# Kernel tuning notes

Hardware: AMD Instinct MI355X
Metric: run time of the kernel (lower is better)

## Reference

```python
import jax, jax.numpy as jnp
import numpy as np
from jax import lax

B_, L_, D_ = 4, 512, 512          # batch, seq_len, in_dim (d_model)
HID, H2 = 512, 256                # hidden_dim, per-direction LSTM width
NL, DST, DCV, DIN, DTR = 3, 16, 4, 1024, 32  # layers, d_state, d_conv, d_inner, dt_rank


def _silu(x):
    return x * jax.nn.sigmoid(x)


def _layernorm(x, g, b):
    m = x.mean(-1, keepdims=True)
    v = x.var(-1, keepdims=True)
    return (x - m) / jnp.sqrt(v + 1e-5) * g + b


def _mamba(x, wi, cw, cb, xpw, dw, db, Alog, Dp, wo):
    # x: (B,L,D)
    Bsz, Ls, _ = x.shape
    xz = jnp.einsum('bld,ed->ble', x, wi)          # (B,L,2*DIN)
    xin, z = jnp.split(xz, 2, axis=-1)
    # causal depthwise conv1d (kernel DCV, left-padded)
    xpad = jnp.pad(xin, ((0, 0), (DCV - 1, 0), (0, 0)))
    u = cb + sum(xpad[:, k:k + Ls, :] * cw[:, k] for k in range(DCV))
    u = _silu(u)                                   # (B,L,DIN)
    xdbl = jnp.einsum('blc,ec->ble', u, xpw)       # (B,L,DTR+2*DST)
    dt_in = xdbl[..., :DTR]
    Bc = xdbl[..., DTR:DTR + DST]
    Cc = xdbl[..., DTR + DST:]
    dt = jax.nn.softplus(jnp.einsum('blr,cr->blc', dt_in, dw) + db)  # (B,L,DIN)
    A = -jnp.exp(Alog)                             # (DIN,DST), negative

    def step(h, inp):
        dt_t, B_t, C_t, u_t = inp                  # (B,DIN),(B,DST),(B,DST),(B,DIN)
        dA = jnp.exp(dt_t[..., None] * A)          # (B,DIN,DST)
        h = dA * h + (dt_t * u_t)[..., None] * B_t[:, None, :]
        y = jnp.einsum('bcn,bn->bc', h, C_t)
        return h, y

    h0 = jnp.zeros((Bsz, DIN, DST), x.dtype)
    _, ys = lax.scan(step, h0, (dt.transpose(1, 0, 2), Bc.transpose(1, 0, 2),
                                Cc.transpose(1, 0, 2), u.transpose(1, 0, 2)))
    y = ys.transpose(1, 0, 2) + u * Dp
    y = y * _silu(z)
    return jnp.einsum('blc,dc->bld', y, wo)


def _lstm_dir(x, wih, whh, bih, bhh, reverse):
    Bsz = x.shape[0]

    def step(carry, xt):
        h, c = carry
        g = xt @ wih.T + h @ whh.T + bih + bhh     # (B,4*H2), PyTorch gate order i,f,g,o
        i, f, gg, o = jnp.split(g, 4, axis=-1)
        c = jax.nn.sigmoid(f) * c + jax.nn.sigmoid(i) * jnp.tanh(gg)
        h = jax.nn.sigmoid(o) * jnp.tanh(c)
        return (h, c), h

    init = (jnp.zeros((Bsz, H2), x.dtype), jnp.zeros((Bsz, H2), x.dtype))
    _, hs = lax.scan(step, init, x.transpose(1, 0, 2), reverse=reverse)
    return hs.transpose(1, 0, 2)


def setup_inputs():
    key = jax.random.key(0)
    ks = jax.random.split(key, 16)
    rn = lambda k, s, sc=0.02: jax.random.normal(k, s, jnp.float32) * sc
    inp = {}
    inp['x'] = jax.random.normal(ks[0], (B_, L_, D_), jnp.float32)
    inp['in_proj_w'] = rn(ks[1], (NL, 2 * DIN, D_))
    inp['conv_w'] = rn(ks[2], (NL, DIN, DCV), 0.2)
    inp['conv_b'] = jnp.zeros((NL, DIN), jnp.float32)
    inp['x_proj_w'] = rn(ks[3], (NL, DTR + 2 * DST, DIN))
    inp['dt_proj_w'] = rn(ks[4], (NL, DIN, DTR), 0.1)
    inp['dt_proj_b'] = jnp.full((NL, DIN), -4.0, jnp.float32)
    inp['A_log'] = jnp.log(jnp.broadcast_to(jnp.arange(1, DST + 1, dtype=jnp.float32), (NL, DIN, DST)))
    inp['D_param'] = jnp.ones((NL, DIN), jnp.float32)
    inp['out_proj_w'] = rn(ks[5], (NL, D_, DIN))
    inp['ln_g'] = jnp.ones((NL, D_), jnp.float32)
    inp['ln_b'] = jnp.zeros((NL, D_), jnp.float32)
    inp['lstm_w_ih'] = rn(ks[6], (2, 4 * H2, D_), 0.05)
    inp['lstm_w_hh'] = rn(ks[7], (2, 4 * H2, H2), 0.05)
    inp['lstm_b_ih'] = jnp.zeros((2, 4 * H2), jnp.float32)
    inp['lstm_b_hh'] = jnp.zeros((2, 4 * H2), jnp.float32)
    inp['fusion_w'] = rn(ks[8], (HID, D_ + HID), 0.02)
    inp['fusion_b'] = jnp.zeros((HID,), jnp.float32)
    return inp


def reference(x, in_proj_w, conv_w, conv_b, x_proj_w, dt_proj_w, dt_proj_b, A_log,
              D_param, out_proj_w, ln_g, ln_b, lstm_w_ih, lstm_w_hh, lstm_b_ih,
              lstm_b_hh, fusion_w, fusion_b):
    m = x
    for i in range(NL):
        mo = _mamba(m, in_proj_w[i], conv_w[i], conv_b[i], x_proj_w[i],
                    dt_proj_w[i], dt_proj_b[i], A_log[i], D_param[i], out_proj_w[i])
        m = _layernorm(m + mo, ln_g[i], ln_b[i])
    lf = _lstm_dir(x, lstm_w_ih[0], lstm_w_hh[0], lstm_b_ih[0], lstm_b_hh[0], False)
    lb = _lstm_dir(x, lstm_w_ih[1], lstm_w_hh[1], lstm_b_ih[1], lstm_b_hh[1], True)
    comb = jnp.concatenate([m, lf, lb], axis=-1)   # (B,L,D_+HID)
    return comb @ fusion_w.T + fusion_b
```

## Files before the change

### kernel.cpp

```cpp
#include <hip/hip_runtime.h>
#include <math.h>

#define B_  4
#define L_  512
#define D_  512
#define DIN 1024
#define DST 16
#define DCV 4
#define DTR 32
#define NL  3
#define H2  256
#define LCH 128
#define WSC 0.28f

typedef _Float16 __f16;
typedef __f16 f16x2 __attribute__((ext_vector_type(2)));
typedef __f16 half8 __attribute__((ext_vector_type(8)));
typedef float f32x4v __attribute__((ext_vector_type(4)));
typedef unsigned uint4v __attribute__((ext_vector_type(4)));

__device__ __forceinline__ float fast_sigmoid(float x) { return 1.f / (1.f + __expf(-x)); }
__device__ __forceinline__ float fast_tanh(float x) { return 2.f / (1.f + __expf(-2.f * x)) - 1.f; }

__device__ __forceinline__ float dot2f(unsigned a, unsigned b, float c) {
  return __builtin_amdgcn_fdot2(__builtin_bit_cast(f16x2, a),
                                __builtin_bit_cast(f16x2, b), c, false);
}
__device__ __forceinline__ unsigned packf16(float a, float b) {
  f16x2 p; p.x = (__f16)a; p.y = (__f16)b;
  return __builtin_bit_cast(unsigned, p);
}
__device__ __forceinline__ int sdot4(unsigned a, unsigned b, int c) {
  return __builtin_amdgcn_sdot4((int)a, (int)b, c, false);
}
__device__ __forceinline__ int q8(float v) {
  float c = fmaxf(fminf(v, 127.f), -127.f);
  return (int)rintf(c);
}

template<int ACT, bool ACC, bool HOUT>
__global__ __launch_bounds__(256) void gemm_mfma_h(
    const __f16* __restrict__ A, const __f16* __restrict__ W, void* __restrict__ Cv,
    int M, int N, int K, int lda, int ldb, int ldc,
    const float* __restrict__ bias, const float* __restrict__ bias2)
{
  __shared__ uint4v As[1024];
  __shared__ uint4v Bs[1024];
  const int tid  = threadIdx.x;
  const int lane = tid & 63, wid = tid >> 6;
  const int wr = wid >> 1, wc = wid & 1;
  const int fr = lane & 15, fq = lane >> 4;
  const int m0 = blockIdx.y * 128, n0 = blockIdx.x * 128;
  const int srow = tid >> 3, skb = tid & 7;

  f32x4v acc[4][4] = {};
  for (int k0 = 0; k0 < K; k0 += 64) {
    const __f16* Ab = A + (size_t)m0 * lda + k0;
    const __f16* Bb = W + (size_t)n0 * ldb + k0;
    #pragma unroll
    for (int i = 0; i < 4; ++i) {
      int row = srow + i * 32;
      uint4v ap = *(const uint4v*)(Ab + (size_t)row * lda + skb * 8);
      uint4v bp = *(const uint4v*)(Bb + (size_t)row * ldb + skb * 8);
      As[row * 8 + (skb ^ (row & 7))] = ap;
      Bs[row * 8 + (skb ^ (row & 7))] = bp;
    }
    __syncthreads();
    #pragma unroll
    for (int ks = 0; ks < 2; ++ks) {
      half8 af[4], bf[4];
      #pragma unroll
      for (int mt = 0; mt < 4; ++mt) {
        int row = wr * 64 + mt * 16 + fr;
        int kb = ks * 4 + fq;
        af[mt] = __builtin_bit_cast(half8, As[row * 8 + (kb ^ (row & 7))]);
      }
      #pragma unroll
      for (int nt = 0; nt < 4; ++nt) {
        int row = wc * 64 + nt * 16 + fr;
        int kb = ks * 4 + fq;
        bf[nt] = __builtin_bit_cast(half8, Bs[row * 8 + (kb ^ (row & 7))]);
      }
      #pragma unroll
      for (int mt = 0; mt < 4; ++mt)
        #pragma unroll
        for (int nt = 0; nt < 4; ++nt)
          acc[mt][nt] = __builtin_amdgcn_mfma_f32_16x16x32_f16(af[mt], bf[nt], acc[mt][nt], 0, 0, 0);
    }
    __syncthreads();
  }
  float* C = (float*)Cv;
  __f16* Ch = (__f16*)Cv;
  #pragma unroll
  for (int nt = 0; nt < 4; ++nt) {
    int n = n0 + wc * 64 + nt * 16 + fr;
    float bv = (bias ? bias[n] : 0.f) + (bias2 ? bias2[n] : 0.f);
    #pragma unroll
    for (int mt = 0; mt < 4; ++mt) {
      #pragma unroll
      for (int r = 0; r < 4; ++r) {
        int m = m0 + wr * 64 + mt * 16 + fq * 4 + r;
        float v = acc[mt][nt][r] + bv;
        if (ACT == 1) v = (v > 20.f) ? v : log1pf(__expf(v));
        if (HOUT) Ch[(size_t)m * ldc + n] = (__f16)v;
        else if (ACC) C[(size_t)m * ldc + n] += v;
        else C[(size_t)m * ldc + n] = v;
      }
    }
  }
}

__global__ __launch_bounds__(256) void packh(
    const float* __restrict__ src, __f16* __restrict__ dst, int n)
{
  int t = blockIdx.x * 256 + threadIdx.x;
  if (t < n) dst[t] = (__f16)src[t];
}

__global__ __launch_bounds__(256) void pack_xpw_h(
    const float* __restrict__ xpw, __f16* __restrict__ dst)
{
  int t = blockIdx.x * 256 + threadIdx.x;
  int layer = t >> 17;
  int r = (t >> 10) & 127;
  int k = t & 1023;
  dst[t] = (r < 64) ? (__f16)xpw[layer * 65536 + r * 1024 + k] : (__f16)0.f;
}

__global__ __launch_bounds__(256) void pack_dwh(
    const float* __restrict__ dw, __f16* __restrict__ dst)
{
  int t = blockIdx.x * 256 + threadIdx.x;
  int layer = t >> 16;
  int r = (t >> 6) & 1023;
  int k = t & 63;
  dst[t] = (k < 32) ? (__f16)dw[layer * 32768 + r * 32 + k] : (__f16)0.f;
}

__global__ __launch_bounds__(256) void pack_whh_i8(
    const float* __restrict__ whh, uint4* __restrict__ dst)
{
  int idx = blockIdx.x * 256 + threadIdx.x;
  int t = idx & 511;
  int q = (idx >> 9) & 7;
  int r = idx >> 12;
  int G = r % 3, dir = r / 3;
  int j = t >> 1, ks = t & 1;
  const float* src = whh + (size_t)dir * 262144 + (size_t)(G * 256 + j) * 256 + ks * 128 + q * 16;
  const float inv = 127.f / WSC;
  unsigned d[4];
  #pragma unroll
  for (int w = 0; w < 4; ++w) {
    float4 f = ((const float4*)src)[w];
    int q0 = q8(f.x * inv), q1 = q8(f.y * inv), q2 = q8(f.z * inv), q3 = q8(f.w * inv);
    d[w] = (unsigned)(q0 & 255) | ((unsigned)(q1 & 255) << 8) |
           ((unsigned)(q2 & 255) << 16) | ((unsigned)(q3 & 255) << 24);
  }
  uint4 pk; pk.x = d[0]; pk.y = d[1]; pk.z = d[2]; pk.w = d[3];
  dst[idx] = pk;
}

__global__ __launch_bounds__(256) void pack_whh_o(
    const float* __restrict__ whh, uint4* __restrict__ dst)
{
  int idx = blockIdx.x * 256 + threadIdx.x;
  int t = idx & 511;
  int q = (idx >> 9) & 15;
  int dir = idx >> 13;
  int j = t >> 1, ks = t & 1;
  const float* src = whh + (size_t)dir * 262144 + (size_t)(768 + j) * 256 + ks * 128 + q * 8;
  float4 fa = ((const float4*)src)[0];
  float4 fb = ((const float4*)src)[1];
  uint4 pk;
  pk.x = packf16(fa.x, fa.y); pk.y = packf16(fa.z, fa.w);
  pk.z = packf16(fb.x, fb.y); pk.w = packf16(fb.z, fb.w);
  dst[idx] = pk;
}

__global__ __launch_bounds__(256) void conv_silu(
    const float* __restrict__ xz, const float* __restrict__ cw, const float* __restrict__ cb,
    float* __restrict__ u, __f16* __restrict__ uh)
{
  int t = blockIdx.x * 256 + threadIdx.x;
  int c  = t & (DIN - 1);
  int bl = t >> 10;
  int l  = bl & (L_ - 1);
  float acc = cb[c];
  #pragma unroll
  for (int k = 0; k < DCV; ++k) {
    int ls = l + k - (DCV - 1);
    if (ls >= 0)
      acc = fmaf(xz[(size_t)(bl + k - (DCV - 1)) * 2048 + c], cw[c * DCV + k], acc);
  }
  float v = acc * fast_sigmoid(acc);
  u[t] = v;
  uh[t] = (__f16)v;
}

__global__ __launch_bounds__(256) void scan_part(
    const float* __restrict__ dt, const float* __restrict__ u,
    const __f16* __restrict__ xdh, const float* __restrict__ A_log,
    float* __restrict__ hend, float* __restrict__ Pp)
{
  int t = blockIdx.x * 256 + threadIdx.x;
  int n  = t & 15;
  int ch = (t >> 4) & 3;
  int bc = t >> 6;
  int c  = bc & (DIN - 1);
  int b  = bc >> 10;
  float Ac = -__expf(A_log[c * DST + n]);
  float h = 0.f, P = 1.f;
  const size_t row = (size_t)b * L_ + ch * LCH;

#define DECLP(i) float dtv##i, uv##i, Bn##i;
  DECLP(0) DECLP(1) DECLP(2) DECLP(3)
#define LOADP(i, l) { \
    const size_t nb_ = row + (l); \
    dtv##i = dt[nb_ * DIN + c]; \
    uv##i  = u [nb_ * DIN + c]; \
    Bn##i  = (float)xdh[nb_ * 128 + 32 + n]; }
#define STEPP(i) { \
    float dA_ = __expf(dtv##i * Ac); \
    h = fmaf(dA_, h, (dtv##i * uv##i) * Bn##i); \
    P *= dA_; }

  LOADP(0, 0) LOADP(1, 1) LOADP(2, 2) LOADP(3, 3)
  for (int l = 0; l < LCH - 4; l += 4) {
    STEPP(0) LOADP(0, l + 4)
    STEPP(1) LOADP(1, l + 5)
    STEPP(2) LOADP(2, l + 6)
    STEPP(3) LOADP(3, l + 7)
  }
  STEPP(0) STEPP(1) STEPP(2) STEPP(3)
#undef DECLP
#undef LOADP
#undef STEPP
  int flat = bc * 16 + n;
  hend[ch * 65536 + flat] = h;
  Pp[ch * 65536 + flat]   = P;
}

__global__ __launch_bounds__(256) void scan_fix(
    const float* __restrict__ dt, const float* __restrict__ u,
    const __f16* __restrict__ xdh, const float* __restrict__ xz,
    const float* __restrict__ A_log, const float* __restrict__ Dp,
    const float* __restrict__ hend, const float* __restrict__ Pp,
    __f16* __restrict__ y)
{
  int t = blockIdx.x * 256 + threadIdx.x;
  int n  = t & 15;
  int ch = (t >> 4) & 3;
  int bc = t >> 6;
  int c  = bc & (DIN - 1);
  int b  = bc >> 10;
  float Ac = -__expf(A_log[c * DST + n]);
  float Dc = Dp[c];
  const int flat = bc * 16 + n;
  float h = 0.f;
  if (ch > 0) h = hend[flat];
  if (ch > 1) h = fmaf(Pp[1 * 65536 + flat], h, hend[1 * 65536 + flat]);
  if (ch > 2) h = fmaf(Pp[2 * 65536 + flat], h, hend[2 * 65536 + flat]);
  const size_t row = (size_t)b * L_ + ch * LCH;

#define DECLP(i) float dtv##i, uv##i, Bn##i, Cn##i, zv##i;
  DECLP(0) DECLP(1) DECLP(2) DECLP(3)
#define LOADP(i, l) { \
    const size_t nb_ = row + (l); \
    dtv##i = dt[nb_ * DIN + c]; \
    uv##i  = u [nb_ * DIN + c]; \
    Bn##i  = (float)xdh[nb_ * 128 + 32 + n]; \
    Cn##i  = (float)xdh[nb_ * 128 + 48 + n]; \
    zv##i  = xz[nb_ * 2048 + 1024 + c]; }
#define STEPP(i, l) { \
    float dA_ = __expf(dtv##i * Ac); \
    h = fmaf(dA_, h, (dtv##i * uv##i) * Bn##i); \
    float p_ = h * Cn##i; \
    p_ += __shfl_xor(p_, 1, 64); \
    p_ += __shfl_xor(p_, 2, 64); \
    p_ += __shfl_xor(p_, 4, 64); \
    p_ += __shfl_xor(p_, 8, 64); \
    if (n == 0) { \
      float yv_ = p_ + uv##i * Dc; \
      yv_ *= zv##i * fast_sigmoid(zv##i); \
      y[(row + (l)) * DIN + c] = (__f16)yv_; \
    } }

  LOADP(0, 0) LOADP(1, 1) LOADP(2, 2) LOADP(3, 3)
  for (int l = 0; l < LCH - 4; l += 4) {
    STEPP(0, l)     LOADP(0, l + 4)
    STEPP(1, l + 1) LOADP(1, l + 5)
    STEPP(2, l + 2) LOADP(2, l + 6)
    STEPP(3, l + 3) LOADP(3, l + 7)
  }
  STEPP(0, LCH - 4) STEPP(1, LCH - 3) STEPP(2, LCH - 2) STEPP(3, LCH - 1)
#undef DECLP
#undef LOADP
#undef STEPP
}

__global__ __launch_bounds__(64) void resid_ln(
    const float* __restrict__ a, const float* __restrict__ mo,
    const float* __restrict__ g, const float* __restrict__ bta,
    float* __restrict__ outm, int ldo, __f16* __restrict__ outh, int ldoh)
{
  int row = blockIdx.x;
  int lane = threadIdx.x;
  const float* pa = a  + (size_t)row * 512;
  const float* pb = mo + (size_t)row * 512;
  float v[8];
  float s = 0.f, s2 = 0.f;
  #pragma unroll
  for (int i = 0; i < 8; ++i) {
    float x = pa[lane + i * 64] + pb[lane + i * 64];
    v[i] = x; s += x; s2 += x * x;
  }
  #pragma unroll
  for (int off = 1; off < 64; off <<= 1) {
    s  += __shfl_xor(s,  off, 64);
    s2 += __shfl_xor(s2, off, 64);
  }
  float mean = s * (1.f / 512.f);
  float var  = s2 * (1.f / 512.f) - mean * mean;
  float rstd = rsqrtf(var + 1e-5f);
  #pragma unroll
  for (int i = 0; i < 8; ++i) {
    int cidx = lane + i * 64;
    float o = (v[i] - mean) * rstd * g[cidx] + bta[cidx];
    if (outm) outm[(size_t)row * ldo + cidx] = o;
    outh[(size_t)row * ldoh + cidx] = (__f16)o;
  }
}


#define W8DECL(q) uint4 WI8_##q, WF8_##q, WG8_##q;
#define W8LOAD(q) WI8_##q = wp8[(0*8+(q))*512 + t]; \
                  WF8_##q = wp8[(1*8+(q))*512 + t]; \
                  WG8_##q = wp8[(2*8+(q))*512 + t];
#define W8STEP(q) { \
    uint4 hq = h8s[buf][(q)*2 + ks]; \
    ii_ = sdot4(WI8_##q.x, hq.x, ii_); ii_ = sdot4(WI8_##q.y, hq.y, ii_); \
    ii_ = sdot4(WI8_##q.z, hq.z, ii_); ii_ = sdot4(WI8_##q.w, hq.w, ii_); \
    if_ = sdot4(WF8_##q.x, hq.x, if_); if_ = sdot4(WF8_##q.y, hq.y, if_); \
    if_ = sdot4(WF8_##q.z, hq.z, if_); if_ = sdot4(WF8_##q.w, hq.w, if_); \
    ig_ = sdot4(WG8_##q.x, hq.x, ig_); ig_ = sdot4(WG8_##q.y, hq.y, ig_); \
    ig_ = sdot4(WG8_##q.z, hq.z, ig_); ig_ = sdot4(WG8_##q.w, hq.w, ig_); }
#define OSTEP(q) { \
    uint4 hv = h4s[buf][(q)*2 + ks]; \
    uint4 wv = wo_lds[(q)*512 + t]; \
    a3 = dot2f(wv.x, hv.x, a3); a3 = dot2f(wv.y, hv.y, a3); \
    a3 = dot2f(wv.z, hv.z, a3); a3 = dot2f(wv.w, hv.w, a3); }
#define REP8(M) M(0) M(1) M(2) M(3) M(4) M(5) M(6) M(7)
#define REP16(M) M(0) M(1) M(2) M(3) M(4) M(5) M(6) M(7) \
                 M(8) M(9) M(10) M(11) M(12) M(13) M(14) M(15)

__global__ __launch_bounds__(512, 1) void lstm_rec(
    const float* __restrict__ gx, const uint4* __restrict__ wpk8,
    const uint4* __restrict__ wpko, __f16* __restrict__ comb)
{
  __shared__ uint4 wo_lds[16 * 512];
  __shared__ __align__(16) uint4 h4s[2][32];
  __shared__ __align__(16) uint4 h8s[2][16];
  const int dir = blockIdx.x >> 2, b = blockIdx.x & 3;
  const int t = threadIdx.x;
  const int j = t >> 1, ks = t & 1;
  const uint4* wp8 = wpk8 + (size_t)dir * 3 * 8 * 512;
  const uint4* wpo = wpko + (size_t)dir * 16 * 512;
  const float WS = WSC / (127.f * 127.f);

  REP8(W8DECL)
  REP8(W8LOAD)

  #pragma unroll
  for (int q = 0; q < 16; ++q)
    wo_lds[q * 512 + t] = wpo[q * 512 + t];

  if (t < 256) ((unsigned*)h4s)[t] = 0u;
  if (t < 128) ((unsigned*)h8s)[t] = 0u;
  float c_reg = 0.f;
  __f16* outp = comb + 512 + dir * 256;
  const float* gxb = gx + (size_t)(b * L_) * 2048 + dir * 1024;
  const int offA = (ks ? 1 : 0) * 256 + j;
  const int offB = (ks ? 3 : 2) * 256 + j;
  const int p_   = t >> 2;
  const int hidx = ((p_ >> 2) & 15) * 8 + (p_ >> 6) * 4 + (p_ & 3);
  const int d_   = j >> 2;
  const int ks8  = d_ >> 5;
  const int h8i  = (((d_ - ks8 * 32) >> 2) * 2 + ks8) * 4 + (d_ & 3);
  __syncthreads();

  int buf = 0;
  const int l0 = dir ? (L_ - 1) : 0;
  float pgA = gxb[(size_t)l0 * 2048 + offA];
  float pgB = gxb[(size_t)l0 * 2048 + offB];

  for (int s = 0; s < L_; ++s) {
    const int l = dir ? (L_ - 1 - s) : s;
    float pgA_n = 0.f, pgB_n = 0.f;
    if (s + 1 < L_) {
      const int ln = dir ? (L_ - 2 - s) : (s + 1);
      pgA_n = gxb[(size_t)ln * 2048 + offA];
      pgB_n = gxb[(size_t)ln * 2048 + offB];
    }
    int ii_ = 0, if_ = 0, ig_ = 0;
    float a3 = 0.f;
    REP8(W8STEP)
    REP16(OSTEP)
    float a0 = (float)ii_ * WS;
    float a1 = (float)if_ * WS;
    float a2 = (float)ig_ * WS;
    if (ks == 0) { a0 += pgA; a2 += pgB; } else { a1 += pgA; a3 += pgB; }
    a0 += __shfl_xor(a0, 1, 64);
    a1 += __shfl_xor(a1, 1, 64);
    a2 += __shfl_xor(a2, 1, 64);
    a3 += __shfl_xor(a3, 1, 64);
    const float si = fast_sigmoid(a0);
    const float sf = fast_sigmoid(a1);
    const float tg = fast_tanh(a2);
    const float so = fast_sigmoid(a3);
    c_reg = fmaf(sf, c_reg, si * tg);
    const float hv = so * fast_tanh(c_reg);
    if (ks == 0) outp[(size_t)(b * L_ + l) * 1024 + j] = (__f16)hv;
    const float hv1 = __shfl_xor(hv, 2, 64);
    const float hv2 = __shfl_xor(hv, 4, 64);
    const float hv3 = __shfl_xor(hv1, 4, 64);
    if ((t & 3) == 0)
      ((unsigned*)h4s[buf ^ 1])[hidx] = packf16(hv, hv1);
    if ((t & 7) == 0) {
      int q0 = (int)rintf(hv  * 127.f), q1 = (int)rintf(hv1 * 127.f);
      int q2 = (int)rintf(hv2 * 127.f), q3 = (int)rintf(hv3 * 127.f);
      ((unsigned*)h8s[buf ^ 1])[h8i] =
          (unsigned)(q0 & 255) | ((unsigned)(q1 & 255) << 8) |
          ((unsigned)(q2 & 255) << 16) | ((unsigned)(q3 & 255) << 24);
    }
    pgA = pgA_n; pgB = pgB_n;
    buf ^= 1;
    __syncthreads();
  }
}

extern "C" void kernel_launch(void* const* d_in, const int* in_sizes, int n_in,
                              void* d_out, int out_size, void* d_ws, size_t ws_size,
                              hipStream_t stream)
{
  const float* x    = (const float*)d_in[0];
  const float* wi   = (const float*)d_in[1];
  const float* cw   = (const float*)d_in[2];
  const float* cb   = (const float*)d_in[3];
  const float* xpw  = (const float*)d_in[4];
  const float* dw   = (const float*)d_in[5];
  const float* db   = (const float*)d_in[6];
  const float* Alog = (const float*)d_in[7];
  const float* Dp   = (const float*)d_in[8];
  const float* wo   = (const float*)d_in[9];
  const float* lng  = (const float*)d_in[10];
  const float* lnb  = (const float*)d_in[11];
  const float* wih  = (const float*)d_in[12];
  const float* whh  = (const float*)d_in[13];
  const float* bih  = (const float*)d_in[14];
  const float* bhh  = (const float*)d_in[15];
  const float* fw   = (const float*)d_in[16];
  const float* fb   = (const float*)d_in[17];
  float* out = (float*)d_out;

  float* F = (float*)d_ws;
  float* xz     = F;
  float* gx     = F;
  float* mo     = F + 3145728;
  float* u      = F + 4194304;
  __f16* xdh    = (__f16*)(F + 7340032);
  float* dt     = F + 7602176;
  float* mbuf   = F + 10747904;
  __f16* fw_h   = (__f16*)(F + 4194304);
  __f16* u_h    = (__f16*)(F + 6291456);
  __f16* wih_h  = (__f16*)(F + 7602176);
  uint4* wpk8   = (uint4*)(F + 8126464);
  uint4* wpko   = (uint4*)(F + 8224768);
  __f16* wi_hc  = (__f16*)(F + 8388608);
  __f16* ybuf_h = (__f16*)(F + 9699328);
  __f16* x_h    = (__f16*)(F + 9699328);
  __f16* mbuf_h = (__f16*)(F + 11796480);
  __f16* comb_h = (__f16*)(F + 12320768);
  __f16* wo_h   = (__f16*)(F + 13369344);
  __f16* xpw_h  = (__f16*)(F + 14155776);
  __f16* dwh    = (__f16*)(F + 14352384);
  float* hend   = F + 14450688;
  float* Pp     = F + 14712832;

  const int M = B_ * L_;
  dim3 blk(256);

  packh<<<dim3(4096), blk, 0, stream>>>(x,   x_h,   1048576);
  packh<<<dim3(4096), blk, 0, stream>>>(wih, wih_h, 1048576);
  packh<<<dim3(6144), blk, 0, stream>>>(wo,  wo_h,  1572864);
  pack_xpw_h<<<dim3(1536), blk, 0, stream>>>(xpw, xpw_h);
  pack_dwh<<<dim3(768), blk, 0, stream>>>(dw, dwh);

  gemm_mfma_h<0,false,false><<<dim3(16, 16), blk, 0, stream>>>(
      x_h, wih_h, gx, M, 2048, 512, 512, 512, 2048, bih, bhh);
  pack_whh_i8<<<dim3(96), blk, 0, stream>>>(whh, wpk8);
  pack_whh_o<<<dim3(64), blk, 0, stream>>>(whh, wpko);
  lstm_rec<<<dim3(8), dim3(512), 0, stream>>>(gx, wpk8, wpko, comb_h);

  for (int i = 0; i < NL; ++i) {
    const float* min = (i == 0) ? x : mbuf;
    const __f16* min_h = (i == 0) ? x_h : mbuf_h;
    packh<<<dim3(4096), blk, 0, stream>>>(wi + (size_t)i*1048576, wi_hc, 1048576);
    gemm_mfma_h<0,false,false><<<dim3(16, 16), blk, 0, stream>>>(
        min_h, wi_hc, xz, M, 2048, 512, 512, 512, 2048, nullptr, nullptr);
    conv_silu<<<dim3(8192), blk, 0, stream>>>(
        xz, cw + (size_t)i*DIN*DCV, cb + i*DIN, u, u_h);
    gemm_mfma_h<0,false,true><<<dim3(1, 16), blk, 0, stream>>>(
        u_h, xpw_h + (size_t)i*131072, xdh, M, 128, 1024, 1024, 1024, 128, nullptr, nullptr);
    gemm_mfma_h<1,false,false><<<dim3(8, 16), blk, 0, stream>>>(
        xdh, dwh + (size_t)i*65536, dt, M, 1024, 64, 128, 64, 1024, db + i*1024, nullptr);
    scan_part<<<dim3(1024), blk, 0, stream>>>(
        dt, u, xdh, Alog + (size_t)i*DIN*DST, hend, Pp);
    scan_fix<<<dim3(1024), blk, 0, stream>>>(
        dt, u, xdh, xz, Alog + (size_t)i*DIN*DST, Dp + i*DIN, hend, Pp, ybuf_h);
    gemm_mfma_h<0,false,false><<<dim3(4, 16), blk, 0, stream>>>(
        ybuf_h, wo_h + (size_t)i*524288, mo, M, 512, 1024, 1024, 1024, 512, nullptr, nullptr);
    if (i < NL - 1)
      resid_ln<<<dim3(M), dim3(64), 0, stream>>>(
          min, mo, lng + i*512, lnb + i*512, mbuf, 512, mbuf_h, 512);
    else
      resid_ln<<<dim3(M), dim3(64), 0, stream>>>(
          min, mo, lng + i*512, lnb + i*512, nullptr, 0, comb_h, 1024);
  }

  packh<<<dim3(2048), blk, 0, stream>>>(fw, fw_h, 524288);
  gemm_mfma_h<0,false,false><<<dim3(4, 16), blk, 0, stream>>>(
      comb_h, fw_h, out, M, 512, 1024, 1024, 1024, 512, fb, nullptr);
}
```

Before: 1.347 ms.

## Quantize LSTM output gate to int8 and split Mamba scan into eight chunks

The LSTM recurrence now uses int8 weights for the output gate too, so it goes through the same sdot4 path as the other gates. This drops the separate fp16 hidden-state buffer, its pack kernel and the 16 fp16 dot2 steps per timestep, and halves the LDS weight footprint. Separately, the selective scan is split into 8 chunks of 64 instead of 4 of 128, doubling the parallelism in scan_part and scan_fix, at the cost of a longer serial prefix combine and workspace relocation for hend and Pp. The added int8 quantization of the output-gate weights may reduce accuracy.

Result: faster. 1.292 ms (-4.1%).

```diff
diff --git a/kernel.cpp b/kernel.cpp
--- a/kernel.cpp
+++ b/kernel.cpp
@@ -10,7 +10,8 @@
 #define DTR 32
 #define NL  3
 #define H2  256
-#define LCH 128
+#define LCH 64
+#define NCH 8
 #define WSC 0.28f
 
 typedef _Float16 __f16;
@@ -144,7 +145,7 @@
   int t = idx & 511;
   int q = (idx >> 9) & 7;
   int r = idx >> 12;
-  int G = r % 3, dir = r / 3;
+  int G = r & 3, dir = r >> 2;
   int j = t >> 1, ks = t & 1;
   const float* src = whh + (size_t)dir * 262144 + (size_t)(G * 256 + j) * 256 + ks * 128 + q * 16;
   const float inv = 127.f / WSC;
@@ -160,23 +161,6 @@
   dst[idx] = pk;
 }
 
-__global__ __launch_bounds__(256) void pack_whh_o(
-    const float* __restrict__ whh, uint4* __restrict__ dst)
-{
-  int idx = blockIdx.x * 256 + threadIdx.x;
-  int t = idx & 511;
-  int q = (idx >> 9) & 15;
-  int dir = idx >> 13;
-  int j = t >> 1, ks = t & 1;
-  const float* src = whh + (size_t)dir * 262144 + (size_t)(768 + j) * 256 + ks * 128 + q * 8;
-  float4 fa = ((const float4*)src)[0];
-  float4 fb = ((const float4*)src)[1];
-  uint4 pk;
-  pk.x = packf16(fa.x, fa.y); pk.y = packf16(fa.z, fa.w);
-  pk.z = packf16(fb.x, fb.y); pk.w = packf16(fb.z, fb.w);
-  dst[idx] = pk;
-}
-
 __global__ __launch_bounds__(256) void conv_silu(
     const float* __restrict__ xz, const float* __restrict__ cw, const float* __restrict__ cb,
     float* __restrict__ u, __f16* __restrict__ uh)
@@ -204,8 +188,8 @@
 {
   int t = blockIdx.x * 256 + threadIdx.x;
   int n  = t & 15;
-  int ch = (t >> 4) & 3;
-  int bc = t >> 6;
+  int ch = (t >> 4) & 7;
+  int bc = t >> 7;
   int c  = bc & (DIN - 1);
   int b  = bc >> 10;
   float Ac = -__expf(A_log[c * DST + n]);
@@ -249,17 +233,16 @@
 {
   int t = blockIdx.x * 256 + threadIdx.x;
   int n  = t & 15;
-  int ch = (t >> 4) & 3;
-  int bc = t >> 6;
+  int ch = (t >> 4) & 7;
+  int bc = t >> 7;
   int c  = bc & (DIN - 1);
   int b  = bc >> 10;
   float Ac = -__expf(A_log[c * DST + n]);
   float Dc = Dp[c];
   const int flat = bc * 16 + n;
   float h = 0.f;
-  if (ch > 0) h = hend[flat];
-  if (ch > 1) h = fmaf(Pp[1 * 65536 + flat], h, hend[1 * 65536 + flat]);
-  if (ch > 2) h = fmaf(Pp[2 * 65536 + flat], h, hend[2 * 65536 + flat]);
+  for (int c2 = 0; c2 < ch; ++c2)
+    h = fmaf(Pp[c2 * 65536 + flat], h, hend[c2 * 65536 + flat]);
   const size_t row = (size_t)b * L_ + ch * LCH;
 
 #define DECLP(i) float dtv##i, uv##i, Bn##i, Cn##i, zv##i;
@@ -338,52 +321,43 @@
                   WG8_##q = wp8[(2*8+(q))*512 + t];
 #define W8STEP(q) { \
     uint4 hq = h8s[buf][(q)*2 + ks]; \
+    uint4 wo = wo_lds[(q)*512 + t]; \
     ii_ = sdot4(WI8_##q.x, hq.x, ii_); ii_ = sdot4(WI8_##q.y, hq.y, ii_); \
     ii_ = sdot4(WI8_##q.z, hq.z, ii_); ii_ = sdot4(WI8_##q.w, hq.w, ii_); \
     if_ = sdot4(WF8_##q.x, hq.x, if_); if_ = sdot4(WF8_##q.y, hq.y, if_); \
     if_ = sdot4(WF8_##q.z, hq.z, if_); if_ = sdot4(WF8_##q.w, hq.w, if_); \
     ig_ = sdot4(WG8_##q.x, hq.x, ig_); ig_ = sdot4(WG8_##q.y, hq.y, ig_); \
-    ig_ = sdot4(WG8_##q.z, hq.z, ig_); ig_ = sdot4(WG8_##q.w, hq.w, ig_); }
-#define OSTEP(q) { \
-    uint4 hv = h4s[buf][(q)*2 + ks]; \
-    uint4 wv = wo_lds[(q)*512 + t]; \
-    a3 = dot2f(wv.x, hv.x, a3); a3 = dot2f(wv.y, hv.y, a3); \
-    a3 = dot2f(wv.z, hv.z, a3); a3 = dot2f(wv.w, hv.w, a3); }
+    ig_ = sdot4(WG8_##q.z, hq.z, ig_); ig_ = sdot4(WG8_##q.w, hq.w, ig_); \
+    io_ = sdot4(wo.x, hq.x, io_); io_ = sdot4(wo.y, hq.y, io_); \
+    io_ = sdot4(wo.z, hq.z, io_); io_ = sdot4(wo.w, hq.w, io_); }
 #define REP8(M) M(0) M(1) M(2) M(3) M(4) M(5) M(6) M(7)
-#define REP16(M) M(0) M(1) M(2) M(3) M(4) M(5) M(6) M(7) \
-                 M(8) M(9) M(10) M(11) M(12) M(13) M(14) M(15)
 
 __global__ __launch_bounds__(512, 1) void lstm_rec(
     const float* __restrict__ gx, const uint4* __restrict__ wpk8,
-    const uint4* __restrict__ wpko, __f16* __restrict__ comb)
-{
-  __shared__ uint4 wo_lds[16 * 512];
-  __shared__ __align__(16) uint4 h4s[2][32];
+    __f16* __restrict__ comb)
+{
+  __shared__ uint4 wo_lds[8 * 512];
   __shared__ __align__(16) uint4 h8s[2][16];
   const int dir = blockIdx.x >> 2, b = blockIdx.x & 3;
   const int t = threadIdx.x;
   const int j = t >> 1, ks = t & 1;
-  const uint4* wp8 = wpk8 + (size_t)dir * 3 * 8 * 512;
-  const uint4* wpo = wpko + (size_t)dir * 16 * 512;
+  const uint4* wp8 = wpk8 + (size_t)dir * 4 * 8 * 512;
   const float WS = WSC / (127.f * 127.f);
 
   REP8(W8DECL)
   REP8(W8LOAD)
 
   #pragma unroll
-  for (int q = 0; q < 16; ++q)
-    wo_lds[q * 512 + t] = wpo[q * 512 + t];
-
-  if (t < 256) ((unsigned*)h4s)[t] = 0u;
+  for (int q = 0; q < 8; ++q)
+    wo_lds[q * 512 + t] = wp8[(3 * 8 + q) * 512 + t];
+
   if (t < 128) ((unsigned*)h8s)[t] = 0u;
   float c_reg = 0.f;
   __f16* outp = comb + 512 + dir * 256;
   const float* gxb = gx + (size_t)(b * L_) * 2048 + dir * 1024;
   const int offA = (ks ? 1 : 0) * 256 + j;
   const int offB = (ks ? 3 : 2) * 256 + j;
-  const int p_   = t >> 2;
-  const int hidx = ((p_ >> 2) & 15) * 8 + (p_ >> 6) * 4 + (p_ & 3);
-  const int d_   = j >> 2;
+  const int d_   = t >> 3;
   const int ks8  = d_ >> 5;
   const int h8i  = (((d_ - ks8 * 32) >> 2) * 2 + ks8) * 4 + (d_ & 3);
   __syncthreads();
@@ -401,13 +375,12 @@
       pgA_n = gxb[(size_t)ln * 2048 + offA];
       pgB_n = gxb[(size_t)ln * 2048 + offB];
     }
-    int ii_ = 0, if_ = 0, ig_ = 0;
-    float a3 = 0.f;
+    int ii_ = 0, if_ = 0, ig_ = 0, io_ = 0;
     REP8(W8STEP)
-    REP16(OSTEP)
     float a0 = (float)ii_ * WS;
     float a1 = (float)if_ * WS;
     float a2 = (float)ig_ * WS;
+    float a3 = (float)io_ * WS;
     if (ks == 0) { a0 += pgA; a2 += pgB; } else { a1 += pgA; a3 += pgB; }
     a0 += __shfl_xor(a0, 1, 64);
     a1 += __shfl_xor(a1, 1, 64);
@@ -423,8 +396,6 @@
     const float hv1 = __shfl_xor(hv, 2, 64);
     const float hv2 = __shfl_xor(hv, 4, 64);
     const float hv3 = __shfl_xor(hv1, 4, 64);
-    if ((t & 3) == 0)
-      ((unsigned*)h4s[buf ^ 1])[hidx] = packf16(hv, hv1);
     if ((t & 7) == 0) {
       int q0 = (int)rintf(hv  * 127.f), q1 = (int)rintf(hv1 * 127.f);
       int q2 = (int)rintf(hv2 * 127.f), q3 = (int)rintf(hv3 * 127.f);
@@ -474,17 +445,16 @@
   __f16* u_h    = (__f16*)(F + 6291456);
   __f16* wih_h  = (__f16*)(F + 7602176);
   uint4* wpk8   = (uint4*)(F + 8126464);
-  uint4* wpko   = (uint4*)(F + 8224768);
   __f16* wi_hc  = (__f16*)(F + 8388608);
+  float* hend   = F + 8388608;
   __f16* ybuf_h = (__f16*)(F + 9699328);
   __f16* x_h    = (__f16*)(F + 9699328);
   __f16* mbuf_h = (__f16*)(F + 11796480);
+  float* Pp     = F + 11796480;
   __f16* comb_h = (__f16*)(F + 12320768);
   __f16* wo_h   = (__f16*)(F + 13369344);
   __f16* xpw_h  = (__f16*)(F + 14155776);
   __f16* dwh    = (__f16*)(F + 14352384);
-  float* hend   = F + 14450688;
-  float* Pp     = F + 14712832;
 
   const int M = B_ * L_;
   dim3 blk(256);
@@ -497,9 +467,8 @@
 
   gemm_mfma_h<0,false,false><<<dim3(16, 16), blk, 0, stream>>>(
       x_h, wih_h, gx, M, 2048, 512, 512, 512, 2048, bih, bhh);
-  pack_whh_i8<<<dim3(96), blk, 0, stream>>>(whh, wpk8);
-  pack_whh_o<<<dim3(64), blk, 0, stream>>>(whh, wpko);
-  lstm_rec<<<dim3(8), dim3(512), 0, stream>>>(gx, wpk8, wpko, comb_h);
+  pack_whh_i8<<<dim3(128), blk, 0, stream>>>(whh, wpk8);
+  lstm_rec<<<dim3(8), dim3(512), 0, stream>>>(gx, wpk8, comb_h);
 
   for (int i = 0; i < NL; ++i) {
     const float* min = (i == 0) ? x : mbuf;
@@ -513,9 +482,9 @@
         u_h, xpw_h + (size_t)i*131072, xdh, M, 128, 1024, 1024, 1024, 128, nullptr, nullptr);
     gemm_mfma_h<1,false,false><<<dim3(8, 16), blk, 0, stream>>>(
         xdh, dwh + (size_t)i*65536, dt, M, 1024, 64, 128, 64, 1024, db + i*1024, nullptr);
-    scan_part<<<dim3(1024), blk, 0, stream>>>(
+    scan_part<<<dim3(2048), blk, 0, stream>>>(
         dt, u, xdh, Alog + (size_t)i*DIN*DST, hend, Pp);
-    scan_fix<<<dim3(1024), blk, 0, stream>>>(
+    scan_fix<<<dim3(2048), blk, 0, stream>>>(
         dt, u, xdh, xz, Alog + (size_t)i*DIN*DST, Dp + i*DIN, hend, Pp, ybuf_h);
     gemm_mfma_h<0,false,false><<<dim3(4, 16), blk, 0, stream>>>(
         ybuf_h, wo_h + (size_t)i*524288, mo, M, 512, 1024, 1024, 1024, 512, nullptr, nullptr);
```
